# Optimization experiments

Hardware: AMD Instinct MI355X
Metric: run time of the kernel (lower is better)

The kernel has to match this reference:

```python
import jax, jax.numpy as jnp
import numpy as np

N, E, D, H = 100000, 600000, 128, 512  # nodes, edges, latent_dim, 4*latent_dim


def setup_inputs() -> dict:
    key = jax.random.key(0)
    ks = jax.random.split(key, 9)
    s = 0.05
    return {
        "z": jax.random.normal(ks[0], (N, D), dtype=jnp.float32),
        "edge_index": jax.random.randint(ks[1], (2, E), 0, N, dtype=jnp.int64),
        "Wg": jax.random.normal(ks[2], (D, D), dtype=jnp.float32) * s,
        "Ws": jax.random.normal(ks[3], (D, D), dtype=jnp.float32) * s,
        "bg": jnp.zeros((D,), dtype=jnp.float32),
        "W1": jax.random.normal(ks[4], (D, H), dtype=jnp.float32) * s,
        "b1": jnp.zeros((H,), dtype=jnp.float32),
        "W2": jax.random.normal(ks[5], (H, H), dtype=jnp.float32) * s,
        "b2": jnp.zeros((H,), dtype=jnp.float32),
        "W3": jax.random.normal(ks[6], (H, D), dtype=jnp.float32) * s,
        "b3": jnp.zeros((D,), dtype=jnp.float32),
    }


def reference(z, edge_index, Wg, Ws, bg, W1, b1, W2, b2, W3, b3):
    src, dst = edge_index[0], edge_index[1]
    n = z.shape[0]
    # GNN: gather neighbor features along edges, mean-aggregate at dst
    msgs = z[src]                                   # (E, D) gather
    agg = jax.ops.segment_sum(msgs, dst, num_segments=n)  # (N, D) scatter-add
    deg = jax.ops.segment_sum(jnp.ones((src.shape[0],), z.dtype), dst, num_segments=n)
    agg = agg / jnp.maximum(deg, 1.0)[:, None]      # mean aggregation
    h = jax.nn.relu(agg @ Wg + z @ Ws + bg)          # (N, D) graph conv output
    # MLP: Linear -> Tanh -> Linear -> Tanh -> Linear
    h = jnp.tanh(h @ W1 + b1)
    h = jnp.tanh(h @ W2 + b2)
    return h @ W3 + b3                               # dz/dt: (N, D)
```

## Files before the change

kernel.cpp:

```cpp
#include <hip/hip_runtime.h>
#include <hip/hip_fp16.h>


typedef _Float16 f16;
typedef __attribute__((ext_vector_type(4))) _Float16 f16x4;
typedef __attribute__((ext_vector_type(8))) _Float16 f16x8;
typedef __attribute__((ext_vector_type(4))) float f32x4;

__device__ __forceinline__ void async_load16(const void* g, void* lds) {
  __builtin_amdgcn_global_load_lds(
      (const __attribute__((address_space(1))) void*)g,
      (__attribute__((address_space(3))) void*)lds, 16, 0, 0);
}

__device__ __forceinline__ float fast_tanh(float x) {
  float a = fabsf(x);
  float e = __expf(-2.0f * a);
  float r = (1.0f - e) * __builtin_amdgcn_rcpf(1.0f + e);
  return copysignf(r, x);
}

__global__ __launch_bounds__(256) void zero_kernel(int* __restrict__ p, int n) {
  int i = blockIdx.x * 256 + threadIdx.x;
  int stride = gridDim.x * 256;
  for (; i < n; i += stride) p[i] = 0;
}

__global__ __launch_bounds__(256) void scan_partial(const int* __restrict__ degi,
                                                    int* __restrict__ bsum, int N) {
  __shared__ int lds[256];
  int b = blockIdx.x, t = threadIdx.x;
  int s = 0;
#pragma unroll
  for (int j = 0; j < 4; ++j) {
    int idx = b * 1024 + t * 4 + j;
    if (idx < N) s += degi[idx];
  }
  lds[t] = s;
  __syncthreads();
  for (int off = 128; off > 0; off >>= 1) {
    if (t < off) lds[t] += lds[t + off];
    __syncthreads();
  }
  if (t == 0) bsum[b] = lds[0];
}

__global__ void scan_bsums(const int* __restrict__ bsum, int* __restrict__ boff,
                           int* __restrict__ row_start, int nb, int N) {
  if (threadIdx.x == 0 && blockIdx.x == 0) {
    int acc = 0;
    for (int i = 0; i < nb; ++i) { boff[i] = acc; acc += bsum[i]; }
    row_start[N] = acc;
  }
}

__global__ __launch_bounds__(256) void scan_final(
    const int* __restrict__ degi, const int* __restrict__ boff,
    int* __restrict__ row_start, int* __restrict__ cursor, int N) {
  __shared__ int lds[256];
  int b = blockIdx.x, t = threadIdx.x;
  int base = b * 1024;
  int v[4];
  int s = 0;
#pragma unroll
  for (int j = 0; j < 4; ++j) {
    int idx = base + t * 4 + j;
    v[j] = (idx < N) ? degi[idx] : 0;
    s += v[j];
  }
  lds[t] = s;
  __syncthreads();
  for (int off = 1; off < 256; off <<= 1) {
    int x = lds[t];
    int y = (t >= off) ? lds[t - off] : 0;
    __syncthreads();
    lds[t] = x + y;
    __syncthreads();
  }
  int pre = boff[b] + lds[t] - s;
#pragma unroll
  for (int j = 0; j < 4; ++j) {
    int idx = base + t * 4 + j;
    if (idx < N) { row_start[idx] = pre; cursor[idx] = pre; pre += v[j]; }
  }
}

__global__ __launch_bounds__(256) void fill_adj(const int* __restrict__ src,
                                                const int* __restrict__ dst,
                                                int* __restrict__ cursor,
                                                int* __restrict__ adj, int E) {
  int e = blockIdx.x * 256 + threadIdx.x;
  if (e >= E) return;
  int p = atomicAdd(&cursor[dst[e]], 1);
  adj[p] = src[e];
}

__global__ __launch_bounds__(256) void fused_prep(
    const int* __restrict__ dst, int* __restrict__ degi, int E,
    const float* __restrict__ Wg, const float* __restrict__ Ws,
    const float* __restrict__ W1, const float* __restrict__ W2,
    const float* __restrict__ W3, f16* __restrict__ wgs, f16* __restrict__ wt1,
    f16* __restrict__ wt2, f16* __restrict__ wt3,
    const float* __restrict__ z, f16* __restrict__ z16, f16* __restrict__ Xc,
    int n4) {
  int i0 = blockIdx.x * 256 + threadIdx.x;
  int stride = gridDim.x * 256;
  for (int i = i0; i < n4; i += stride) {
    float4 v = *(const float4*)(z + 4 * (long long)i);
    f16x4 c;
    c[0] = (f16)v.x; c[1] = (f16)v.y; c[2] = (f16)v.z; c[3] = (f16)v.w;
    *(f16x4*)(z16 + 4 * (long long)i) = c;
    int node = i >> 5, sl = i & 31;
    *(f16x4*)(Xc + (long long)node * 256 + 128 + 4 * sl) = c;
  }
  for (int i = i0; i < E; i += stride) atomicAdd(&degi[dst[i]], 1);
  for (int i = i0; i < 425984; i += stride) {
    if (i < 32768) {
      int n = i >> 8, k = i & 255;
      wgs[i] = (f16)((k < 128) ? Wg[k * 128 + n] : Ws[(k - 128) * 128 + n]);
    } else if (i < 98304) {
      int j = i - 32768, c = j >> 7, k = j & 127;
      wt1[j] = (f16)W1[k * 512 + c];
    } else if (i < 360448) {
      int j = i - 98304, c = j >> 9, k = j & 511;
      wt2[j] = (f16)W2[k * 512 + c];
    } else {
      int j = i - 360448, c = j >> 9, k = j & 511;
      wt3[j] = (f16)W3[k * 128 + c];
    }
  }
}

__global__ __launch_bounds__(256) void gather_xcat(
    const f16* __restrict__ z16, const int* __restrict__ row_start,
    const int* __restrict__ adj, f16* __restrict__ Xc, int N) {
  int node = (blockIdx.x * 256 + threadIdx.x) >> 5;
  if (node >= N) return;
  int lane = threadIdx.x & 31;
  int beg = row_start[node], end = row_start[node + 1];
  float a0 = 0, a1 = 0, a2 = 0, a3 = 0;
#pragma unroll
  for (int j = 0; j < 8; ++j) {
    int idx = beg + j;
    bool vld = idx < end;
    int nb = vld ? adj[idx] : node;
    f16x4 x = *(const f16x4*)(z16 + (long long)nb * 128 + 4 * lane);
    float w = vld ? 1.0f : 0.0f;
    a0 += w * (float)x[0]; a1 += w * (float)x[1];
    a2 += w * (float)x[2]; a3 += w * (float)x[3];
  }
  int i = beg + 8;
  if (i < end) {
    float b0 = 0, b1 = 0, b2 = 0, b3 = 0;
    float c0 = 0, c1 = 0, c2 = 0, c3 = 0;
    float d0 = 0, d1 = 0, d2 = 0, d3 = 0;
    for (; i + 4 <= end; i += 4) {
      int n0 = adj[i], n1 = adj[i + 1], n2 = adj[i + 2], n3 = adj[i + 3];
      f16x4 v0 = *(const f16x4*)(z16 + (long long)n0 * 128 + 4 * lane);
      f16x4 v1 = *(const f16x4*)(z16 + (long long)n1 * 128 + 4 * lane);
      f16x4 v2 = *(const f16x4*)(z16 + (long long)n2 * 128 + 4 * lane);
      f16x4 v3 = *(const f16x4*)(z16 + (long long)n3 * 128 + 4 * lane);
      a0 += (float)v0[0]; a1 += (float)v0[1]; a2 += (float)v0[2]; a3 += (float)v0[3];
      b0 += (float)v1[0]; b1 += (float)v1[1]; b2 += (float)v1[2]; b3 += (float)v1[3];
      c0 += (float)v2[0]; c1 += (float)v2[1]; c2 += (float)v2[2]; c3 += (float)v2[3];
      d0 += (float)v3[0]; d1 += (float)v3[1]; d2 += (float)v3[2]; d3 += (float)v3[3];
    }
    for (; i < end; ++i) {
      f16x4 v = *(const f16x4*)(z16 + (long long)adj[i] * 128 + 4 * lane);
      a0 += (float)v[0]; a1 += (float)v[1]; a2 += (float)v[2]; a3 += (float)v[3];
    }
    a0 += b0 + c0 + d0; a1 += b1 + c1 + d1;
    a2 += b2 + c2 + d2; a3 += b3 + c3 + d3;
  }
  int dg = end - beg;
  float inv = 1.0f / (float)(dg > 1 ? dg : 1);
  long long o = (long long)node * 256;
  f16x4 m;
  m[0] = (f16)(a0 * inv); m[1] = (f16)(a1 * inv);
  m[2] = (f16)(a2 * inv); m[3] = (f16)(a3 * inv);
  *(f16x4*)(Xc + o + 4 * lane) = m;
}

template <int K, int NOUT, int WM, int WN, int MI, int ACT, bool OUTF32>
__global__ __launch_bounds__(WM * WN * 64) void gemm_r(
    const f16* __restrict__ X, const f16* __restrict__ Wt,
    const float* __restrict__ bias, void* __restrict__ OutV, int M) {
  constexpr int NJ = 4;
  constexpr int BM = WM * MI * 16;
  constexpr int BN = WN * NJ * 16;
  constexpr int NTHR = WM * WN * 64;
  constexpr int CA = (BM * 128) / (NTHR * 16);
  constexpr int CB = (BN * 128) / (NTHR * 16);
  __shared__ __align__(16) f16 As[BM * 64];
  __shared__ __align__(16) f16 Bs[BN * 64];

  const int tid = threadIdx.x;
  const int wid = tid >> 6, lane = tid & 63;
  const int wm = wid / WN, wn = wid % WN;
  const int lr = lane & 15, lq = lane >> 4;
  const int rxor = lr & 7;
  const long long m0 = (long long)blockIdx.x * BM;
  const int n0 = blockIdx.y * BN;

  const f16* Ag = X + m0 * K;
  const f16* Bg = Wt + (long long)n0 * K;

  long long aOff[CA], bOff[CB];
#pragma unroll
  for (int c = 0; c < CA; ++c) {
    int f = c * NTHR + tid;
    int row = f >> 3, ss = (f & 7) ^ (row & 7);
    aOff[c] = (long long)row * K + ss * 8;
  }
#pragma unroll
  for (int c = 0; c < CB; ++c) {
    int f = c * NTHR + tid;
    int row = f >> 3, ss = (f & 7) ^ (row & 7);
    bOff[c] = (long long)row * K + ss * 8;
  }

  f32x4 acc[MI][NJ];
#pragma unroll
  for (int i = 0; i < MI; ++i)
#pragma unroll
    for (int j = 0; j < NJ; ++j)
#pragma unroll
      for (int r = 0; r < 4; ++r) acc[i][j][r] = 0.0f;

#pragma unroll 1
  for (int k0 = 0; k0 < K; k0 += 64) {
#pragma unroll
    for (int c = 0; c < CA; ++c)
      async_load16(Ag + aOff[c] + k0, (char*)As + c * NTHR * 16 + wid * 1024);
#pragma unroll
    for (int c = 0; c < CB; ++c)
      async_load16(Bg + bOff[c] + k0, (char*)Bs + c * NTHR * 16 + wid * 1024);
    __syncthreads();
#pragma unroll
    for (int kk = 0; kk < 64; kk += 32) {
      const int co = (((kk >> 3) + lq) ^ rxor) * 16;
      f16x8 a[MI], b[NJ];
#pragma unroll
      for (int i = 0; i < MI; ++i)
        a[i] = *reinterpret_cast<const f16x8*>(
            (const char*)As + (wm * MI * 16 + i * 16 + lr) * 128 + co);
#pragma unroll
      for (int j = 0; j < NJ; ++j)
        b[j] = *reinterpret_cast<const f16x8*>(
            (const char*)Bs + (wn * NJ * 16 + j * 16 + lr) * 128 + co);
#pragma unroll
      for (int i = 0; i < MI; ++i)
#pragma unroll
        for (int j = 0; j < NJ; ++j)
          acc[i][j] = __builtin_amdgcn_mfma_f32_16x16x32_f16(a[i], b[j], acc[i][j], 0, 0, 0);
    }
    __syncthreads();
  }

#pragma unroll
  for (int i = 0; i < MI; ++i) {
#pragma unroll
    for (int j = 0; j < NJ; ++j) {
      int col = n0 + wn * NJ * 16 + j * 16 + lr;
      float bv = bias[col];
#pragma unroll
      for (int r = 0; r < 4; ++r) {
        long long row = m0 + wm * MI * 16 + i * 16 + lq * 4 + r;
        if (row < M) {
          float v = acc[i][j][r] + bv;
          if (ACT == 1) v = fmaxf(v, 0.0f);
          else if (ACT == 2) v = fast_tanh(v);
          if constexpr (OUTF32)
            ((float*)OutV)[row * NOUT + col] = v;
          else
            ((f16*)OutV)[row * NOUT + col] = (f16)v;
        }
      }
    }
  }
}

extern "C" void kernel_launch(void* const* d_in, const int* in_sizes, int n_in,
                              void* d_out, int out_size, void* d_ws, size_t ws_size,
                              hipStream_t stream) {
  const float* z  = (const float*)d_in[0];
  const int*   ei = (const int*)d_in[1];
  const float* Wg = (const float*)d_in[2];
  const float* Ws = (const float*)d_in[3];
  const float* bg = (const float*)d_in[4];
  const float* W1 = (const float*)d_in[5];
  const float* b1 = (const float*)d_in[6];
  const float* W2 = (const float*)d_in[7];
  const float* b2 = (const float*)d_in[8];
  const float* W3 = (const float*)d_in[9];
  const float* b3 = (const float*)d_in[10];

  const int Nn = in_sizes[0] / 128;
  const int E  = in_sizes[1] / 2;
  const int* src = ei;
  const int* dst = ei + E;
  const int nb = (Nn + 1023) / 1024;
  const int gm128 = (Nn + 127) / 128;
  const long long Mpad = (long long)gm128 * 128;

  char* base = (char*)d_ws;
  const size_t XCB = (size_t)Mpad * 256 * 2;
  const size_t H1B = (size_t)Mpad * 128 * 2;
  const size_t H3B = (size_t)Mpad * 512 * 2;
  f16* Xc = (f16*)(base);
  f16* h1 = (f16*)(base + XCB);
  f16* h3 = (f16*)(base);
  size_t off = XCB + H1B;
  auto alloc = [&](size_t b) -> void* {
    void* p = base + off;
    off += (b + 255) & ~(size_t)255;
    return p;
  };
  int* degi      = (int*)alloc((size_t)Nn * 4);
  int* row_start = (int*)alloc((size_t)(Nn + 1) * 4);
  int* cursor    = (int*)alloc((size_t)Nn * 4);
  int* adj       = (int*)alloc((size_t)(E + 8) * 4);
  int* bsum      = (int*)alloc((size_t)nb * 4);
  int* boff      = (int*)alloc((size_t)nb * 4);
  f16* z16       = (f16*)alloc((size_t)Nn * 128 * 2);
  off = H3B;
  f16* h2  = (f16*)alloc((size_t)Mpad * 512 * 2);
  f16* wgs = (f16*)alloc((size_t)128 * 256 * 2);
  f16* wt1 = (f16*)alloc((size_t)512 * 128 * 2);
  f16* wt2 = (f16*)alloc((size_t)512 * 512 * 2);
  f16* wt3 = (f16*)alloc((size_t)128 * 512 * 2);

  zero_kernel<<<(Nn + 255) / 256, 256, 0, stream>>>(degi, Nn);
  fused_prep<<<2048, 256, 0, stream>>>(dst, degi, E, Wg, Ws, W1, W2, W3,
                                       wgs, wt1, wt2, wt3, z, z16, Xc, Nn * 32);
  scan_partial<<<nb, 256, 0, stream>>>(degi, bsum, Nn);
  scan_bsums<<<1, 64, 0, stream>>>(bsum, boff, row_start, nb, Nn);
  scan_final<<<nb, 256, 0, stream>>>(degi, boff, row_start, cursor, Nn);
  fill_adj<<<(E + 255) / 256, 256, 0, stream>>>(src, dst, cursor, adj, E);

  {
    long long tot = (long long)Nn * 32;
    gather_xcat<<<(int)((tot + 255) / 256), 256, 0, stream>>>(z16, row_start, adj, Xc, Nn);
  }

  gemm_r<256, 128, 2, 2, 4, 1, false><<<dim3(gm128, 1), 256, 0, stream>>>(Xc, wgs, bg, (void*)h1, Nn);
  gemm_r<128, 512, 2, 4, 4, 2, false><<<dim3(gm128, 2), 512, 0, stream>>>(h1, wt1, b1, (void*)h2, Nn);
  gemm_r<512, 512, 2, 4, 4, 2, false><<<dim3(gm128, 2), 512, 0, stream>>>(h2, wt2, b2, (void*)h3, Nn);
  gemm_r<512, 128, 2, 2, 4, 0, true><<<dim3(gm128, 1), 256, 0, stream>>>(h3, wt3, b3, d_out, Nn);
}
```

Baseline: 329.1 us.

## Fuse second and third MLP GEMMs, keeping tanh activations in LDS

Replaces the separate H×H GEMM (with tanh) and the H×D output GEMM with one kernel. Each 128-row block computes 128-column chunks of the hidden layer, applies bias and tanh, writes the chunk as f16 into swizzled shared memory, and accumulates it straight into the output GEMM. This avoids writing and re-reading the 512-wide intermediate h3 through global memory and drops one launch. In exchange, the grid is halved to one block per 128 rows with 256 threads. Loads are not double-buffered and there are many barriers, so latency hiding and occupancy may suffer.

After: 447.9 us. 1.36x slower.

```diff
diff --git a/kernel.cpp b/kernel.cpp
--- a/kernel.cpp
+++ b/kernel.cpp
@@ -280,6 +280,131 @@
   }
 }
 
+__global__ __launch_bounds__(256) void fused34(
+    const f16* __restrict__ h2, const f16* __restrict__ wt2,
+    const f16* __restrict__ wt3, const float* __restrict__ b2,
+    const float* __restrict__ b3, float* __restrict__ out, int M) {
+  __shared__ __align__(16) char L[49152];
+  const int tid = threadIdx.x;
+  const int wid = tid >> 6, lane = tid & 63;
+  const int wm = wid & 1, wn = wid >> 1;
+  const int lr = lane & 15, lq = lane >> 4;
+  const int key = lr & 7;
+  const long long m0 = (long long)blockIdx.x * 128;
+  const f16* Ag = h2 + m0 * 512;
+
+  long long sOff[4];
+#pragma unroll
+  for (int c = 0; c < 4; ++c) {
+    int f = c * 256 + tid;
+    int row = f >> 3, ss = (f & 7) ^ (row & 7);
+    sOff[c] = (long long)row * 512 + ss * 8;
+  }
+
+  f32x4 oacc[4][4];
+#pragma unroll
+  for (int i = 0; i < 4; ++i)
+#pragma unroll
+    for (int j = 0; j < 4; ++j)
+#pragma unroll
+      for (int r = 0; r < 4; ++r) oacc[i][j][r] = 0.0f;
+
+#pragma unroll 1
+  for (int cb = 0; cb < 4; ++cb) {
+    const f16* Bg = wt2 + (long long)(cb * 128) * 512;
+    f32x4 acc[4][4];
+#pragma unroll
+    for (int i = 0; i < 4; ++i)
+#pragma unroll
+      for (int j = 0; j < 4; ++j)
+#pragma unroll
+        for (int r = 0; r < 4; ++r) acc[i][j][r] = 0.0f;
+
+#pragma unroll 1
+    for (int k0 = 0; k0 < 512; k0 += 64) {
+#pragma unroll
+      for (int c = 0; c < 4; ++c)
+        async_load16(Ag + sOff[c] + k0, L + c * 4096 + wid * 1024);
+#pragma unroll
+      for (int c = 0; c < 4; ++c)
+        async_load16(Bg + sOff[c] + k0, L + 16384 + c * 4096 + wid * 1024);
+      __syncthreads();
+#pragma unroll
+      for (int kk = 0; kk < 64; kk += 32) {
+        const int co = (((kk >> 3) + lq) ^ key) * 16;
+        f16x8 a[4], b[4];
+#pragma unroll
+        for (int i = 0; i < 4; ++i)
+          a[i] = *reinterpret_cast<const f16x8*>(L + (wm * 64 + i * 16 + lr) * 128 + co);
+#pragma unroll
+        for (int j = 0; j < 4; ++j)
+          b[j] = *reinterpret_cast<const f16x8*>(L + 16384 + (wn * 64 + j * 16 + lr) * 128 + co);
+#pragma unroll
+        for (int i = 0; i < 4; ++i)
+#pragma unroll
+          for (int j = 0; j < 4; ++j)
+            acc[i][j] = __builtin_amdgcn_mfma_f32_16x16x32_f16(a[i], b[j], acc[i][j], 0, 0, 0);
+      }
+      __syncthreads();
+    }
+
+#pragma unroll
+    for (int i = 0; i < 4; ++i)
+#pragma unroll
+      for (int j = 0; j < 4; ++j) {
+        int col = wn * 64 + j * 16 + lr;
+        float bv = b2[cb * 128 + col];
+#pragma unroll
+        for (int r = 0; r < 4; ++r) {
+          int row = wm * 64 + i * 16 + lq * 4 + r;
+          *reinterpret_cast<f16*>(L + row * 256 + (((col >> 3) ^ (row & 7)) << 4) +
+                                  (col & 7) * 2) = (f16)fast_tanh(acc[i][j][r] + bv);
+        }
+      }
+    __syncthreads();
+
+#pragma unroll 1
+    for (int ks = 0; ks < 2; ++ks) {
+#pragma unroll
+      for (int c = 0; c < 4; ++c)
+        async_load16(wt3 + sOff[c] + cb * 128 + ks * 64,
+                     L + 32768 + c * 4096 + wid * 1024);
+      __syncthreads();
+#pragma unroll
+      for (int kk = 0; kk < 64; kk += 32) {
+        const int aco = ((ks * 8 + (kk >> 3) + lq) ^ key) * 16;
+        const int bco = (((kk >> 3) + lq) ^ key) * 16;
+        f16x8 a[4], b[4];
+#pragma unroll
+        for (int i = 0; i < 4; ++i)
+          a[i] = *reinterpret_cast<const f16x8*>(L + (wm * 64 + i * 16 + lr) * 256 + aco);
+#pragma unroll
+        for (int j = 0; j < 4; ++j)
+          b[j] = *reinterpret_cast<const f16x8*>(L + 32768 + (wn * 64 + j * 16 + lr) * 128 + bco);
+#pragma unroll
+        for (int i = 0; i < 4; ++i)
+#pragma unroll
+          for (int j = 0; j < 4; ++j)
+            oacc[i][j] = __builtin_amdgcn_mfma_f32_16x16x32_f16(a[i], b[j], oacc[i][j], 0, 0, 0);
+      }
+      __syncthreads();
+    }
+  }
+
+#pragma unroll
+  for (int i = 0; i < 4; ++i)
+#pragma unroll
+    for (int j = 0; j < 4; ++j) {
+      int col = wn * 64 + j * 16 + lr;
+      float bv = b3[col];
+#pragma unroll
+      for (int r = 0; r < 4; ++r) {
+        long long row = m0 + wm * 64 + i * 16 + lq * 4 + r;
+        if (row < M) out[row * 128 + col] = oacc[i][j][r] + bv;
+      }
+    }
+}
+
 extern "C" void kernel_launch(void* const* d_in, const int* in_sizes, int n_in,
                               void* d_out, int out_size, void* d_ws, size_t ws_size,
                               hipStream_t stream) {
@@ -306,10 +431,8 @@
   char* base = (char*)d_ws;
   const size_t XCB = (size_t)Mpad * 256 * 2;
   const size_t H1B = (size_t)Mpad * 128 * 2;
-  const size_t H3B = (size_t)Mpad * 512 * 2;
   f16* Xc = (f16*)(base);
   f16* h1 = (f16*)(base + XCB);
-  f16* h3 = (f16*)(base);
   size_t off = XCB + H1B;
   auto alloc = [&](size_t b) -> void* {
     void* p = base + off;
@@ -323,7 +446,6 @@
   int* bsum      = (int*)alloc((size_t)nb * 4);
   int* boff      = (int*)alloc((size_t)nb * 4);
   f16* z16       = (f16*)alloc((size_t)Nn * 128 * 2);
-  off = H3B;
   f16* h2  = (f16*)alloc((size_t)Mpad * 512 * 2);
   f16* wgs = (f16*)alloc((size_t)128 * 256 * 2);
   f16* wt1 = (f16*)alloc((size_t)512 * 128 * 2);
@@ -345,6 +467,5 @@
 
   gemm_r<256, 128, 2, 2, 4, 1, false><<<dim3(gm128, 1), 256, 0, stream>>>(Xc, wgs, bg, (void*)h1, Nn);
   gemm_r<128, 512, 2, 4, 4, 2, false><<<dim3(gm128, 2), 512, 0, stream>>>(h1, wt1, b1, (void*)h2, Nn);
-  gemm_r<512, 512, 2, 4, 4, 2, false><<<dim3(gm128, 2), 512, 0, stream>>>(h2, wt2, b2, (void*)h3, Nn);
-  gemm_r<512, 128, 2, 2, 4, 0, true><<<dim3(gm128, 1), 256, 0, stream>>>(h3, wt3, b3, d_out, Nn);
-}
+  fused34<<<gm128, 256, 0, stream>>>(h2, wt2, wt3, b2, b3, (float*)d_out, Nn);
+}
```
